# Kernel tuning notes

Measured on AMD Instinct MI355X. Metric: run time of the kernel, lower is better.

The kernel has to match this reference:

```python
import jax, jax.numpy as jnp
import numpy as np
import math

B, S, H = 4, 4096, 64
WINDOW = 2


def setup_inputs() -> dict:
    key = jax.random.key(0)
    ks = jax.random.split(key, 7)
    s = 0.05
    return {
        "feature": jax.random.normal(ks[0], (B, S, H), dtype=jnp.float32),
        "Wq": jax.random.normal(ks[1], (H, H), dtype=jnp.float32) * s,
        "bq": jax.random.normal(ks[2], (H,), dtype=jnp.float32) * s,
        "Wk": jax.random.normal(ks[3], (H, H), dtype=jnp.float32) * s,
        "bk": jax.random.normal(ks[4], (H,), dtype=jnp.float32) * s,
        "Wv": jax.random.normal(ks[5], (H, H), dtype=jnp.float32) * s,
        "bv": jax.random.normal(ks[6], (H,), dtype=jnp.float32) * s,
    }


def reference(feature, Wq, bq, Wk, bk, Wv, bv):
    b, seq, d_k = feature.shape
    # torch nn.Linear: y = x @ W.T + b
    q = feature @ Wq.T + bq  # [B,S,H]
    k = feature @ Wk.T + bk
    v = feature @ Wv.T + bv

    # banded 0/1 mask, |i-j| <= window, then softmax over the FULL row
    # (faithful to the original: zeros outside the band also get exp(0)=1 weight)
    idx = jnp.arange(seq)
    band = (jnp.abs(idx[:, None] - idx[None, :]) <= WINDOW).astype(jnp.float32)  # [S,S]
    weights = jax.nn.softmax(band, axis=-1)  # [S,S]

    # locally-averaged K: weights @ k, shared across batch
    mixed_k = jnp.einsum('st,bth->bsh', weights, k)  # [B,S,H]
    scores = jnp.einsum('bsh,bth->bst', q, mixed_k) / math.sqrt(d_k)  # [B,S,S]
    attn = jax.nn.softmax(scores, axis=-1)
    out = jnp.einsum('bst,bth->bsh', attn, v)  # [B,S,H]
    return out
```

## Files before the change

kernel.cpp:

```cpp
#include <hip/hip_runtime.h>
#include <hip/hip_bf16.h>
#include <math.h>

#define SEQ 4096
#define HD  64
#define NBATCH 4

#define EM1  1.71828182845904523536f
#define INVD5 (1.0f/(4096.f + 5.f*EM1))
#define INVD4 (1.0f/(4096.f + 4.f*EM1))
#define INVD3 (1.0f/(4096.f + 3.f*EM1))

typedef __attribute__((ext_vector_type(8))) short short8;
typedef __attribute__((ext_vector_type(4))) float f32x4;

__device__ __forceinline__ f32x4 mfma16(short8 a, short8 b, f32x4 c) {
    return __builtin_amdgcn_mfma_f32_16x16x32_bf16(a, b, c, 0, 0, 0);
}

__device__ __forceinline__ short bfs(float x) {
    __hip_bfloat16 h = __float2bfloat16(x);
    return *(short*)&h;
}

__device__ __forceinline__ short8 pack8(float4 a, float4 b) {
    short8 r;
    r[0] = bfs(a.x); r[1] = bfs(a.y); r[2] = bfs(a.z); r[3] = bfs(a.w);
    r[4] = bfs(b.x); r[5] = bfs(b.y); r[6] = bfs(b.z); r[7] = bfs(b.w);
    return r;
}

__device__ __forceinline__ float blo(unsigned v) { return __uint_as_float(v << 16); }
__device__ __forceinline__ float bhi(unsigned v) { return __uint_as_float(v & 0xffff0000u); }

__global__ __launch_bounds__(256) void proj_kernel(
    const float* __restrict__ feat,
    const float* __restrict__ Wq, const float* __restrict__ bq,
    const float* __restrict__ Wk, const float* __restrict__ bk,
    const float* __restrict__ Wv, const float* __restrict__ bv,
    __hip_bfloat16* __restrict__ qsb, __hip_bfloat16* __restrict__ ktb,
    __hip_bfloat16* __restrict__ vtb,
    float* __restrict__ kpart, float* __restrict__ vpart)
{
    __shared__ __hip_bfloat16 tscr[64 * 66];
    __shared__ float red[4][64];

    const int tid  = threadIdx.x;
    const int wave = tid >> 6, lane = tid & 63;
    const int quad = lane >> 4, ln = lane & 15;
    const int R0 = blockIdx.x * 64;
    const int b  = R0 >> 12;
    const int t0 = R0 & (SEQ - 1);

    short8 af0, af1;
    {
        const float* fp = feat + (size_t)(R0 + wave * 16 + ln) * HD + quad * 8;
        af0 = pack8(*(const float4*)(fp),      *(const float4*)(fp + 4));
        af1 = pack8(*(const float4*)(fp + 32), *(const float4*)(fp + 36));
    }

    const float* Ws[3] = {Wq, Wk, Wv};
    const float* Bs[3] = {bq, bk, bv};

    #pragma unroll
    for (int m = 0; m < 3; ++m) {
        const float* W = Ws[m];
        const float* bias = Bs[m];
        #pragma unroll
        for (int ct = 0; ct < 4; ++ct) {
            const int col = ct * 16 + ln;
            const float* wp = W + (size_t)col * HD + quad * 8;
            short8 b0 = pack8(*(const float4*)(wp),      *(const float4*)(wp + 4));
            short8 b1 = pack8(*(const float4*)(wp + 32), *(const float4*)(wp + 36));
            f32x4 c = {};
            c = mfma16(af0, b0, c);
            c = mfma16(af1, b1, c);
            const float bl = bias[col];

            if (m == 0) {
                #pragma unroll
                for (int r = 0; r < 4; ++r) {
                    const int row = R0 + wave * 16 + quad * 4 + r;
                    qsb[(size_t)row * HD + col] = __float2bfloat16((c[r] + bl) * 0.125f);
                }
            } else {
                float tot = c[0] + c[1] + c[2] + c[3];
                tot += __shfl_xor(tot, 16);
                tot += __shfl_xor(tot, 32);
                if (quad == 0) red[wave][col] = tot;
                #pragma unroll
                for (int r = 0; r < 4; ++r) {
                    const int rl = wave * 16 + quad * 4 + r;
                    tscr[rl * 66 + col] = __float2bfloat16(c[r] + bl);
                }
            }
        }
        if (m > 0) {
            __syncthreads();
            if (tid < 64) {
                float s = red[0][tid] + red[1][tid] + red[2][tid] + red[3][tid]
                        + 64.f * bias[tid];
                (m == 1 ? kpart : vpart)[(size_t)blockIdx.x * 64 + tid] = s;
            }
            __hip_bfloat16* dst = (m == 1) ? ktb : vtb;
            #pragma unroll
            for (int i = 0; i < 2; ++i) {
                const int tsk = tid + i * 256;
                const int hh = tsk >> 3, c8 = tsk & 7;
                short8 vv;
                #pragma unroll
                for (int j = 0; j < 8; ++j)
                    vv[j] = *(const short*)&tscr[(c8 * 8 + j) * 66 + hh];
                *(short8*)(dst + ((size_t)(b * HD + hh)) * SEQ + t0 + c8 * 8) = vv;
            }
            __syncthreads();
        }
    }
}

__global__ __launch_bounds__(256) void mkernel(
    const __hip_bfloat16* __restrict__ ktb, const __hip_bfloat16* __restrict__ vtb,
    const float* __restrict__ kpart, float* __restrict__ Mpart)
{
    __shared__ float kts[64 * 74];
    __shared__ __hip_bfloat16 mkt[64 * 72];
    __shared__ __hip_bfloat16 vts[64 * 72];
    __shared__ float ktl[64];
    __shared__ float red[4][64];

    const int tid = threadIdx.x;
    const int b = blockIdx.y, chunk = blockIdx.x;
    const int t0 = chunk * 64;
    const int h = tid & 63, g = tid >> 6;

    {
        float kp = 0.f;
        for (int j = g * 16; j < g * 16 + 16; ++j)
            kp += kpart[(size_t)(b * 64 + j) * 64 + h];
        red[g][h] = kp;
    }

    for (int i = tid; i < 64 * 34; i += 256) {
        const int r = i / 34, c = i - r * 34;
        const int gt = t0 - 2 + c * 2;
        unsigned val = 0;
        if (gt >= 0 && gt <= SEQ - 2)
            val = *(const unsigned*)(ktb + (size_t)(b * 64 + r) * SEQ + gt);
        kts[r * 74 + c * 2]     = blo(val);
        kts[r * 74 + c * 2 + 1] = bhi(val);
    }
    for (int i = tid; i < 512; i += 256) {
        const int r = i >> 3, c = i & 7;
        *(uint4*)&vts[r * 72 + c * 8] =
            ((const uint4*)(vtb + (size_t)(b * 64 + r) * SEQ + t0))[c];
    }
    __syncthreads();
    if (tid < 64) ktl[tid] = red[0][tid] + red[1][tid] + red[2][tid] + red[3][tid];
    __syncthreads();

    {
        const int tb = g * 16;
        float w[20];
        #pragma unroll
        for (int j = 0; j < 20; ++j) w[j] = kts[h * 74 + tb + j];
        const float ktv = ktl[h];
        short8 o0, o1;
        #pragma unroll
        for (int i = 0; i < 16; ++i) {
            const int t = t0 + tb + i;
            float invD = INVD5;
            if (t < 2)            invD = (t == 0) ? INVD3 : INVD4;
            else if (t > SEQ - 3) invD = (t == SEQ - 1) ? INVD3 : INVD4;
            const float loc = w[i] + w[i+1] + w[i+2] + w[i+3] + w[i+4];
            const float mkv = (EM1 * loc + ktv) * invD;
            if (i < 8) o0[i] = bfs(mkv); else o1[i - 8] = bfs(mkv);
        }
        *(short8*)&mkt[h * 72 + tb]     = o0;
        *(short8*)&mkt[h * 72 + tb + 8] = o1;
    }
    __syncthreads();

    const int wave = g, lane = tid & 63, quad = lane >> 4, ln = lane & 15;
    f32x4 acc[4] = {};
    #pragma unroll
    for (int ks = 0; ks < 2; ++ks) {
        short8 a = *(const short8*)&mkt[(wave * 16 + ln) * 72 + ks * 32 + quad * 8];
        #pragma unroll
        for (int ct = 0; ct < 4; ++ct) {
            short8 bb = *(const short8*)&vts[(ct * 16 + ln) * 72 + ks * 32 + quad * 8];
            acc[ct] = mfma16(a, bb, acc[ct]);
        }
    }
    const size_t mb = (size_t)(b * 64 + chunk) * 4096;
    #pragma unroll
    for (int ct = 0; ct < 4; ++ct)
        #pragma unroll
        for (int r = 0; r < 4; ++r)
            Mpart[mb + (size_t)(wave * 16 + quad * 4 + r) * 64 + ct * 16 + ln] = acc[ct][r];
}

__global__ __launch_bounds__(256) void mreduce_kernel(
    const float* __restrict__ Mpart, const float* __restrict__ kpart,
    const float* __restrict__ vpart, const __hip_bfloat16* __restrict__ ktb,
    __hip_bfloat16* __restrict__ MT, float* __restrict__ Vtot)
{
    const int b = blockIdx.y, slab = blockIdx.x;
    const int tid = threadIdx.x;
    const int h1 = slab * 4 + (tid >> 6);
    const int h2 = tid & 63;

    float s = 0.f;
    for (int c = 0; c < 64; ++c)
        s += Mpart[(size_t)(b * 64 + c) * 4096 + h1 * 64 + h2];
    MT[(size_t)b * 5120 + h2 * 64 + h1] = __float2bfloat16(s);

    if (slab == 0 && tid < 64) {
        const int hh = tid;
        float kt = 0.f;
        for (int j = 0; j < 64; ++j)
            kt += kpart[(size_t)(b * 64 + j) * 64 + hh];
        const __hip_bfloat16* kr = ktb + (size_t)(b * 64 + hh) * SEQ;
        const float e0 = __bfloat162float(kr[0]), e1 = __bfloat162float(kr[1]);
        const float e2 = __bfloat162float(kr[2]), e3 = __bfloat162float(kr[3]);
        const float f0 = __bfloat162float(kr[SEQ-4]), f1 = __bfloat162float(kr[SEQ-3]);
        const float f2 = __bfloat162float(kr[SEQ-2]), f3 = __bfloat162float(kr[SEQ-1]);
        const float Sint = 5.f*kt - 4.f*e0 - 3.f*e1 - 2.f*e2 - e3
                         - f0 - 2.f*f1 - 3.f*f2 - 4.f*f3;
        const float SlocD = Sint * INVD5
                          + (e0+e1+e2 + f1+f2+f3) * INVD3
                          + (e0+e1+e2+e3 + f0+f1+f2+f3) * INVD4;
        const float mktot = kt * (4092.f*INVD5 + 2.f*INVD4 + 2.f*INVD3) + EM1 * SlocD;
        MT[(size_t)b * 5120 + 64 * 64 + hh] = __float2bfloat16(mktot);
    }
    if (slab == 1 && tid < 64) {
        float s2 = 0.f;
        for (int j = 0; j < 64; ++j)
            s2 += vpart[(size_t)(b * 64 + j) * 64 + tid];
        Vtot[b * 64 + tid] = s2;
    }
    if (slab == 2) {
        for (int i = tid; i < 15 * 64; i += 256)
            MT[(size_t)b * 5120 + 65 * 64 + i] = __float2bfloat16(0.f);
    }
}

__global__ __launch_bounds__(256) void out_kernel(
    const __hip_bfloat16* __restrict__ qsb, const __hip_bfloat16* __restrict__ MT,
    const float* __restrict__ Vtot, float* __restrict__ out)
{
    const int tid = threadIdx.x;
    const int wave = tid >> 6, lane = tid & 63;
    const int quad = lane >> 4, ln = lane & 15;
    const int R0 = blockIdx.x * 64;
    const int b = R0 >> 12;
    const int qrow = R0 + wave * 16;

    short8 qa0, qa1;
    {
        const __hip_bfloat16* qp = qsb + (size_t)(qrow + ln) * HD + quad * 8;
        qa0 = *(const short8*)qp;
        qa1 = *(const short8*)(qp + 32);
    }

    const __hip_bfloat16* mtb = MT + (size_t)b * 5120;
    f32x4 acc[5] = {};
    #pragma unroll
    for (int ct = 0; ct < 5; ++ct) {
        short8 b0 = *(const short8*)(mtb + (ct * 16 + ln) * 64 + quad * 8);
        short8 b1 = *(const short8*)(mtb + (ct * 16 + ln) * 64 + 32 + quad * 8);
        acc[ct] = mfma16(qa0, b0, acc[ct]);
        acc[ct] = mfma16(qa1, b1, acc[ct]);
    }

    float vt[4];
    #pragma unroll
    for (int ct = 0; ct < 4; ++ct) vt[ct] = Vtot[b * 64 + ct * 16 + ln];

    float inv[4];
    #pragma unroll
    for (int r = 0; r < 4; ++r) {
        const float den = __shfl(acc[4][r], lane & 48);
        inv[r] = 1.f / (4096.f + den);
    }
    #pragma unroll
    for (int ct = 0; ct < 4; ++ct)
        #pragma unroll
        for (int r = 0; r < 4; ++r)
            out[(size_t)(qrow + quad * 4 + r) * HD + ct * 16 + ln] =
                (vt[ct] + acc[ct][r]) * inv[r];
}

extern "C" void kernel_launch(void* const* d_in, const int* in_sizes, int n_in,
                              void* d_out, int out_size, void* d_ws, size_t ws_size,
                              hipStream_t stream)
{
    const float* feat = (const float*)d_in[0];
    const float* Wq = (const float*)d_in[1];
    const float* bq = (const float*)d_in[2];
    const float* Wk = (const float*)d_in[3];
    const float* bk = (const float*)d_in[4];
    const float* Wv = (const float*)d_in[5];
    const float* bv = (const float*)d_in[6];
    float* out = (float*)d_out;

    char* ws = (char*)d_ws;
    __hip_bfloat16* qsb   = (__hip_bfloat16*)(ws + 0);
    __hip_bfloat16* ktb   = (__hip_bfloat16*)(ws + (2u << 20));
    __hip_bfloat16* vtb   = (__hip_bfloat16*)(ws + (4u << 20));
    float*          kpart = (float*)(ws + (6u << 20));
    float*          vpart = (float*)(ws + (6u << 20) + 65536);
    float*          Mpart = (float*)(ws + (6u << 20) + 131072);
    __hip_bfloat16* MT    = (__hip_bfloat16*)(ws + (10u << 20) + 131072);
    float*          Vtot  = (float*)(ws + (10u << 20) + 131072 + 40960);

    proj_kernel<<<dim3((NBATCH * SEQ) / 64), dim3(256), 0, stream>>>(
        feat, Wq, bq, Wk, bk, Wv, bv, qsb, ktb, vtb, kpart, vpart);
    mkernel<<<dim3(64, NBATCH), dim3(256), 0, stream>>>(ktb, vtb, kpart, Mpart);
    mreduce_kernel<<<dim3(16, NBATCH), dim3(256), 0, stream>>>(
        Mpart, kpart, vpart, ktb, MT, Vtot);
    out_kernel<<<dim3((NBATCH * SEQ) / 64), dim3(256), 0, stream>>>(
        qsb, MT, Vtot, out);
}
```

Measured before the change: 91.73 us.

## Split all four kernels into finer-grained blocks to raise parallelism

The projection kernel now uses one wave per 16 rows and one projection matrix per grid-y slice, giving 3072 small blocks instead of 256. The M-accumulation kernel halves its time chunk to 32, which doubles its blocks and the partial buffers. The reduction kernel assigns one h1 row per block and splits the chunk sum across four waves. The output kernel uses single-wave blocks. The aim is more concurrent blocks across the many CUs. The cost is extra partial-sum traffic, longer serial reductions over kpart and vpart, and redundant feature loads across the projection slices.

After: 98.58 us. 1.07x slower.

```diff
diff --git a/kernel.cpp b/kernel.cpp
--- a/kernel.cpp
+++ b/kernel.cpp
@@ -33,7 +33,7 @@
 __device__ __forceinline__ float blo(unsigned v) { return __uint_as_float(v << 16); }
 __device__ __forceinline__ float bhi(unsigned v) { return __uint_as_float(v & 0xffff0000u); }
 
-__global__ __launch_bounds__(256) void proj_kernel(
+__global__ __launch_bounds__(64) void proj_kernel(
     const float* __restrict__ feat,
     const float* __restrict__ Wq, const float* __restrict__ bq,
     const float* __restrict__ Wk, const float* __restrict__ bk,
@@ -42,78 +42,73 @@
     __hip_bfloat16* __restrict__ vtb,
     float* __restrict__ kpart, float* __restrict__ vpart)
 {
-    __shared__ __hip_bfloat16 tscr[64 * 66];
-    __shared__ float red[4][64];
+    __shared__ __hip_bfloat16 tscr[16 * 66];
 
     const int tid  = threadIdx.x;
-    const int wave = tid >> 6, lane = tid & 63;
-    const int quad = lane >> 4, ln = lane & 15;
-    const int R0 = blockIdx.x * 64;
+    const int quad = tid >> 4, ln = tid & 15;
+    const int mi = blockIdx.y;
+    const int R0 = blockIdx.x * 16;
     const int b  = R0 >> 12;
     const int t0 = R0 & (SEQ - 1);
 
+    const float* W    = (mi == 0) ? Wq : (mi == 1) ? Wk : Wv;
+    const float* bias = (mi == 0) ? bq : (mi == 1) ? bk : bv;
+
     short8 af0, af1;
     {
-        const float* fp = feat + (size_t)(R0 + wave * 16 + ln) * HD + quad * 8;
+        const float* fp = feat + (size_t)(R0 + ln) * HD + quad * 8;
         af0 = pack8(*(const float4*)(fp),      *(const float4*)(fp + 4));
         af1 = pack8(*(const float4*)(fp + 32), *(const float4*)(fp + 36));
     }
 
-    const float* Ws[3] = {Wq, Wk, Wv};
-    const float* Bs[3] = {bq, bk, bv};
-
-    #pragma unroll
-    for (int m = 0; m < 3; ++m) {
-        const float* W = Ws[m];
-        const float* bias = Bs[m];
-        #pragma unroll
-        for (int ct = 0; ct < 4; ++ct) {
-            const int col = ct * 16 + ln;
-            const float* wp = W + (size_t)col * HD + quad * 8;
-            short8 b0 = pack8(*(const float4*)(wp),      *(const float4*)(wp + 4));
-            short8 b1 = pack8(*(const float4*)(wp + 32), *(const float4*)(wp + 36));
-            f32x4 c = {};
-            c = mfma16(af0, b0, c);
-            c = mfma16(af1, b1, c);
-            const float bl = bias[col];
-
-            if (m == 0) {
-                #pragma unroll
-                for (int r = 0; r < 4; ++r) {
-                    const int row = R0 + wave * 16 + quad * 4 + r;
-                    qsb[(size_t)row * HD + col] = __float2bfloat16((c[r] + bl) * 0.125f);
-                }
-            } else {
-                float tot = c[0] + c[1] + c[2] + c[3];
-                tot += __shfl_xor(tot, 16);
-                tot += __shfl_xor(tot, 32);
-                if (quad == 0) red[wave][col] = tot;
-                #pragma unroll
-                for (int r = 0; r < 4; ++r) {
-                    const int rl = wave * 16 + quad * 4 + r;
-                    tscr[rl * 66 + col] = __float2bfloat16(c[r] + bl);
-                }
+    float colsum[4];
+    #pragma unroll
+    for (int ct = 0; ct < 4; ++ct) {
+        const int col = ct * 16 + ln;
+        const float* wp = W + (size_t)col * HD + quad * 8;
+        short8 b0 = pack8(*(const float4*)(wp),      *(const float4*)(wp + 4));
+        short8 b1 = pack8(*(const float4*)(wp + 32), *(const float4*)(wp + 36));
+        f32x4 c = {};
+        c = mfma16(af0, b0, c);
+        c = mfma16(af1, b1, c);
+        const float bl = bias[col];
+
+        if (mi == 0) {
+            #pragma unroll
+            for (int r = 0; r < 4; ++r)
+                qsb[(size_t)(R0 + quad * 4 + r) * HD + col] =
+                    __float2bfloat16((c[r] + bl) * 0.125f);
+        } else {
+            float tot = c[0] + c[1] + c[2] + c[3];
+            tot += __shfl_xor(tot, 16);
+            tot += __shfl_xor(tot, 32);
+            colsum[ct] = tot;
+            #pragma unroll
+            for (int r = 0; r < 4; ++r)
+                tscr[(quad * 4 + r) * 66 + col] = __float2bfloat16(c[r] + bl);
+        }
+    }
+
+    if (mi != 0) {
+        __syncthreads();
+        float* part = (mi == 1) ? kpart : vpart;
+        if (quad == 0) {
+            #pragma unroll
+            for (int ct = 0; ct < 4; ++ct) {
+                const int col = ct * 16 + ln;
+                part[(size_t)blockIdx.x * 64 + col] = colsum[ct] + 16.f * bias[col];
             }
         }
-        if (m > 0) {
-            __syncthreads();
-            if (tid < 64) {
-                float s = red[0][tid] + red[1][tid] + red[2][tid] + red[3][tid]
-                        + 64.f * bias[tid];
-                (m == 1 ? kpart : vpart)[(size_t)blockIdx.x * 64 + tid] = s;
-            }
-            __hip_bfloat16* dst = (m == 1) ? ktb : vtb;
+        __hip_bfloat16* dst = (mi == 1) ? ktb : vtb;
+        #pragma unroll
+        for (int i = 0; i < 2; ++i) {
+            const int tsk = i * 64 + tid;
+            const int hh = tsk >> 1, c8 = tsk & 1;
+            short8 vv;
             #pragma unroll
-            for (int i = 0; i < 2; ++i) {
-                const int tsk = tid + i * 256;
-                const int hh = tsk >> 3, c8 = tsk & 7;
-                short8 vv;
-                #pragma unroll
-                for (int j = 0; j < 8; ++j)
-                    vv[j] = *(const short*)&tscr[(c8 * 8 + j) * 66 + hh];
-                *(short8*)(dst + ((size_t)(b * HD + hh)) * SEQ + t0 + c8 * 8) = vv;
-            }
-            __syncthreads();
+            for (int j = 0; j < 8; ++j)
+                vv[j] = *(const short*)&tscr[(c8 * 8 + j) * 66 + hh];
+            *(short8*)(dst + ((size_t)(b * HD + hh)) * SEQ + t0 + c8 * 8) = vv;
         }
     }
 }
@@ -122,36 +117,36 @@
     const __hip_bfloat16* __restrict__ ktb, const __hip_bfloat16* __restrict__ vtb,
     const float* __restrict__ kpart, float* __restrict__ Mpart)
 {
-    __shared__ float kts[64 * 74];
-    __shared__ __hip_bfloat16 mkt[64 * 72];
-    __shared__ __hip_bfloat16 vts[64 * 72];
+    __shared__ float kts[64 * 38];
+    __shared__ __hip_bfloat16 mkt[64 * 40];
+    __shared__ __hip_bfloat16 vts[64 * 40];
     __shared__ float ktl[64];
     __shared__ float red[4][64];
 
     const int tid = threadIdx.x;
     const int b = blockIdx.y, chunk = blockIdx.x;
-    const int t0 = chunk * 64;
+    const int t0 = chunk * 32;
     const int h = tid & 63, g = tid >> 6;
 
     {
         float kp = 0.f;
-        for (int j = g * 16; j < g * 16 + 16; ++j)
-            kp += kpart[(size_t)(b * 64 + j) * 64 + h];
+        for (int j = 0; j < 64; ++j)
+            kp += kpart[(size_t)(b * 256 + g * 64 + j) * 64 + h];
         red[g][h] = kp;
     }
 
-    for (int i = tid; i < 64 * 34; i += 256) {
-        const int r = i / 34, c = i - r * 34;
+    for (int i = tid; i < 64 * 18; i += 256) {
+        const int r = i / 18, c = i - r * 18;
         const int gt = t0 - 2 + c * 2;
         unsigned val = 0;
         if (gt >= 0 && gt <= SEQ - 2)
             val = *(const unsigned*)(ktb + (size_t)(b * 64 + r) * SEQ + gt);
-        kts[r * 74 + c * 2]     = blo(val);
-        kts[r * 74 + c * 2 + 1] = bhi(val);
-    }
-    for (int i = tid; i < 512; i += 256) {
-        const int r = i >> 3, c = i & 7;
-        *(uint4*)&vts[r * 72 + c * 8] =
+        kts[r * 38 + c * 2]     = blo(val);
+        kts[r * 38 + c * 2 + 1] = bhi(val);
+    }
+    {
+        const int r = tid >> 2, c = tid & 3;
+        *(uint4*)&vts[r * 40 + c * 8] =
             ((const uint4*)(vtb + (size_t)(b * 64 + r) * SEQ + t0))[c];
     }
     __syncthreads();
@@ -159,39 +154,34 @@
     __syncthreads();
 
     {
-        const int tb = g * 16;
-        float w[20];
-        #pragma unroll
-        for (int j = 0; j < 20; ++j) w[j] = kts[h * 74 + tb + j];
+        const int tb = g * 8;
+        float w[12];
+        #pragma unroll
+        for (int j = 0; j < 12; ++j) w[j] = kts[h * 38 + tb + j];
         const float ktv = ktl[h];
-        short8 o0, o1;
-        #pragma unroll
-        for (int i = 0; i < 16; ++i) {
+        short8 o;
+        #pragma unroll
+        for (int i = 0; i < 8; ++i) {
             const int t = t0 + tb + i;
             float invD = INVD5;
             if (t < 2)            invD = (t == 0) ? INVD3 : INVD4;
             else if (t > SEQ - 3) invD = (t == SEQ - 1) ? INVD3 : INVD4;
             const float loc = w[i] + w[i+1] + w[i+2] + w[i+3] + w[i+4];
-            const float mkv = (EM1 * loc + ktv) * invD;
-            if (i < 8) o0[i] = bfs(mkv); else o1[i - 8] = bfs(mkv);
+            o[i] = bfs((EM1 * loc + ktv) * invD);
         }
-        *(short8*)&mkt[h * 72 + tb]     = o0;
-        *(short8*)&mkt[h * 72 + tb + 8] = o1;
+        *(short8*)&mkt[h * 40 + tb] = o;
     }
     __syncthreads();
 
     const int wave = g, lane = tid & 63, quad = lane >> 4, ln = lane & 15;
+    short8 a = *(const short8*)&mkt[(wave * 16 + ln) * 40 + quad * 8];
     f32x4 acc[4] = {};
     #pragma unroll
-    for (int ks = 0; ks < 2; ++ks) {
-        short8 a = *(const short8*)&mkt[(wave * 16 + ln) * 72 + ks * 32 + quad * 8];
-        #pragma unroll
-        for (int ct = 0; ct < 4; ++ct) {
-            short8 bb = *(const short8*)&vts[(ct * 16 + ln) * 72 + ks * 32 + quad * 8];
-            acc[ct] = mfma16(a, bb, acc[ct]);
-        }
-    }
-    const size_t mb = (size_t)(b * 64 + chunk) * 4096;
+    for (int ct = 0; ct < 4; ++ct) {
+        short8 bb = *(const short8*)&vts[(ct * 16 + ln) * 40 + quad * 8];
+        acc[ct] = mfma16(a, bb, acc[ct]);
+    }
+    const size_t mb = (size_t)(b * 128 + chunk) * 4096;
     #pragma unroll
     for (int ct = 0; ct < 4; ++ct)
         #pragma unroll
@@ -204,21 +194,25 @@
     const float* __restrict__ vpart, const __hip_bfloat16* __restrict__ ktb,
     __hip_bfloat16* __restrict__ MT, float* __restrict__ Vtot)
 {
-    const int b = blockIdx.y, slab = blockIdx.x;
+    __shared__ float red[4][64];
+    const int b = blockIdx.y, h1 = blockIdx.x;
     const int tid = threadIdx.x;
-    const int h1 = slab * 4 + (tid >> 6);
-    const int h2 = tid & 63;
+    const int g = tid >> 6, h2 = tid & 63;
 
     float s = 0.f;
-    for (int c = 0; c < 64; ++c)
-        s += Mpart[(size_t)(b * 64 + c) * 4096 + h1 * 64 + h2];
-    MT[(size_t)b * 5120 + h2 * 64 + h1] = __float2bfloat16(s);
-
-    if (slab == 0 && tid < 64) {
+    for (int c = 0; c < 32; ++c)
+        s += Mpart[(size_t)(b * 128 + g * 32 + c) * 4096 + h1 * 64 + h2];
+    red[g][h2] = s;
+    __syncthreads();
+    if (tid < 64)
+        MT[(size_t)b * 5120 + tid * 64 + h1] =
+            __float2bfloat16(red[0][tid] + red[1][tid] + red[2][tid] + red[3][tid]);
+
+    if (h1 == 0 && tid < 64) {
         const int hh = tid;
         float kt = 0.f;
-        for (int j = 0; j < 64; ++j)
-            kt += kpart[(size_t)(b * 64 + j) * 64 + hh];
+        for (int j = 0; j < 256; ++j)
+            kt += kpart[(size_t)(b * 256 + j) * 64 + hh];
         const __hip_bfloat16* kr = ktb + (size_t)(b * 64 + hh) * SEQ;
         const float e0 = __bfloat162float(kr[0]), e1 = __bfloat162float(kr[1]);
         const float e2 = __bfloat162float(kr[2]), e3 = __bfloat162float(kr[3]);
@@ -232,32 +226,30 @@
         const float mktot = kt * (4092.f*INVD5 + 2.f*INVD4 + 2.f*INVD3) + EM1 * SlocD;
         MT[(size_t)b * 5120 + 64 * 64 + hh] = __float2bfloat16(mktot);
     }
-    if (slab == 1 && tid < 64) {
+    if (h1 == 1 && tid < 64) {
         float s2 = 0.f;
-        for (int j = 0; j < 64; ++j)
-            s2 += vpart[(size_t)(b * 64 + j) * 64 + tid];
+        for (int j = 0; j < 256; ++j)
+            s2 += vpart[(size_t)(b * 256 + j) * 64 + tid];
         Vtot[b * 64 + tid] = s2;
     }
-    if (slab == 2) {
+    if (h1 == 2) {
         for (int i = tid; i < 15 * 64; i += 256)
             MT[(size_t)b * 5120 + 65 * 64 + i] = __float2bfloat16(0.f);
     }
 }
 
-__global__ __launch_bounds__(256) void out_kernel(
+__global__ __launch_bounds__(64) void out_kernel(
     const __hip_bfloat16* __restrict__ qsb, const __hip_bfloat16* __restrict__ MT,
     const float* __restrict__ Vtot, float* __restrict__ out)
 {
     const int tid = threadIdx.x;
-    const int wave = tid >> 6, lane = tid & 63;
-    const int quad = lane >> 4, ln = lane & 15;
-    const int R0 = blockIdx.x * 64;
+    const int quad = tid >> 4, ln = tid & 15;
+    const int R0 = blockIdx.x * 16;
     const int b = R0 >> 12;
-    const int qrow = R0 + wave * 16;
 
     short8 qa0, qa1;
     {
-        const __hip_bfloat16* qp = qsb + (size_t)(qrow + ln) * HD + quad * 8;
+        const __hip_bfloat16* qp = qsb + (size_t)(R0 + ln) * HD + quad * 8;
         qa0 = *(const short8*)qp;
         qa1 = *(const short8*)(qp + 32);
     }
@@ -279,14 +271,14 @@
     float inv[4];
     #pragma unroll
     for (int r = 0; r < 4; ++r) {
-        const float den = __shfl(acc[4][r], lane & 48);
+        const float den = __shfl(acc[4][r], tid & 48);
         inv[r] = 1.f / (4096.f + den);
     }
     #pragma unroll
     for (int ct = 0; ct < 4; ++ct)
         #pragma unroll
         for (int r = 0; r < 4; ++r)
-            out[(size_t)(qrow + quad * 4 + r) * HD + ct * 16 + ln] =
+            out[(size_t)(R0 + quad * 4 + r) * HD + ct * 16 + ln] =
                 (vt[ct] + acc[ct][r]) * inv[r];
 }
 
@@ -308,16 +300,15 @@
     __hip_bfloat16* ktb   = (__hip_bfloat16*)(ws + (2u << 20));
     __hip_bfloat16* vtb   = (__hip_bfloat16*)(ws + (4u << 20));
     float*          kpart = (float*)(ws + (6u << 20));
-    float*          vpart = (float*)(ws + (6u << 20) + 65536);
-    float*          Mpart = (float*)(ws + (6u << 20) + 131072);
-    __hip_bfloat16* MT    = (__hip_bfloat16*)(ws + (10u << 20) + 131072);
-    float*          Vtot  = (float*)(ws + (10u << 20) + 131072 + 40960);
-
-    proj_kernel<<<dim3((NBATCH * SEQ) / 64), dim3(256), 0, stream>>>(
+    float*          vpart = (float*)(ws + (6u << 20) + 262144);
+    float*          Mpart = (float*)(ws + (6u << 20) + 524288);
+    __hip_bfloat16* MT    = (__hip_bfloat16*)(ws + (14u << 20) + 524288);
+    float*          Vtot  = (float*)(ws + (14u << 20) + 524288 + 40960);
+
+    proj_kernel<<<dim3(1024, 3), dim3(64), 0, stream>>>(
         feat, Wq, bq, Wk, bk, Wv, bv, qsb, ktb, vtb, kpart, vpart);
-    mkernel<<<dim3(64, NBATCH), dim3(256), 0, stream>>>(ktb, vtb, kpart, Mpart);
-    mreduce_kernel<<<dim3(16, NBATCH), dim3(256), 0, stream>>>(
+    mkernel<<<dim3(128, NBATCH), dim3(256), 0, stream>>>(ktb, vtb, kpart, Mpart);
+    mreduce_kernel<<<dim3(64, NBATCH), dim3(256), 0, stream>>>(
         Mpart, kpart, vpart, ktb, MT, Vtot);
-    out_kernel<<<dim3((NBATCH * SEQ) / 64), dim3(256), 0, stream>>>(
-        qsb, MT, Vtot, out);
-}
+    out_kernel<<<dim3(1024), dim3(64), 0, stream>>>(qsb, MT, Vtot, out);
+}
```
